# Performance work log

Hardware: AMD Instinct MI355X
Metric: run time of the kernel (lower is better)

Reference implementation:

```python
import jax, jax.numpy as jnp
import numpy as np

WS = 16                     # window_size
OW = 24                     # overlap_win_size = int(16*0.5)+16
PAD = (OW - WS) // 2        # unfold padding = 4
DIM = 384
HEADS = 6
HID = 768                   # mlp_ratio 2.0 * dim
TABLE = (WS + OW - 1) ** 2  # 1521


def _rel_pos_index():
    ch = np.arange(WS)
    coords = np.stack(np.meshgrid(ch, ch, indexing='ij')).reshape(2, -1)      # (2, WS*WS)
    co = np.arange(OW)
    coords_o = np.stack(np.meshgrid(co, co, indexing='ij')).reshape(2, -1)    # (2, OW*OW)
    rel = coords[:, :, None] - coords_o[:, None, :]                           # (2, nq, nk)
    rel = rel.transpose(1, 2, 0).astype(np.int64)
    rel[..., 0] += OW - 1
    rel[..., 1] += OW - 1
    rel[..., 0] *= WS + OW - 1
    return rel.sum(-1)                                                        # (WS*WS, OW*OW)

RPI = jnp.asarray(_rel_pos_index())


def _ln(x, g, b, eps=1e-5):
    m = x.mean(-1, keepdims=True)
    v = ((x - m) ** 2).mean(-1, keepdims=True)
    return (x - m) / jnp.sqrt(v + eps) * g + b


def _overlap_windows(t, H, W):
    # t: (B,H,W,C) -> (B*nw, OW*OW, C); overlapping patches, stride WS, pad PAD
    B, _, _, C = t.shape
    nH, nW = H // WS, W // WS
    tp = jnp.pad(t, ((0, 0), (PAD, PAD), (PAD, PAD), (0, 0)))
    r = (jnp.arange(nH) * WS)[:, None] + jnp.arange(OW)   # (nH, OW)
    c = (jnp.arange(nW) * WS)[:, None] + jnp.arange(OW)   # (nW, OW)
    p = tp[:, r]              # (B, nH, OW, Wp, C)
    p = p[:, :, :, c]         # (B, nH, OW, nW, OW, C)
    p = p.transpose(0, 1, 3, 2, 4, 5).reshape(B * nH * nW, OW * OW, C)
    return p


def setup_inputs() -> dict:
    key = jax.random.key(0)
    ks = jax.random.split(key, 8)
    H = W = 192
    B = 1
    inp = {
        'x': jax.random.normal(ks[0], (B, H * W, DIM), dtype=jnp.float32),
        'norm1_g': jnp.ones((DIM,), jnp.float32),
        'norm1_b': jnp.zeros((DIM,), jnp.float32),
        'qkv_w': jax.random.normal(ks[1], (DIM, 3 * DIM), jnp.float32) * 0.02,
        'qkv_b': jnp.zeros((3 * DIM,), jnp.float32),
        'rpb_table': jax.random.normal(ks[2], (TABLE, HEADS), jnp.float32) * 0.02,
        'proj_w': jax.random.normal(ks[3], (DIM, DIM), jnp.float32) * 0.02,
        'proj_b': jnp.zeros((DIM,), jnp.float32),
        'norm2_g': jnp.ones((DIM,), jnp.float32),
        'norm2_b': jnp.zeros((DIM,), jnp.float32),
        'fc1_w': jax.random.normal(ks[4], (DIM, HID), jnp.float32) * 0.02,
        'fc1_b': jnp.zeros((HID,), jnp.float32),
        'fc2_w': jax.random.normal(ks[5], (HID, DIM), jnp.float32) * 0.02,
        'fc2_b': jnp.zeros((DIM,), jnp.float32),
        'H': H,
        'W': W,
    }
    return inp


def reference(x, norm1_g, norm1_b, qkv_w, qkv_b, rpb_table, proj_w, proj_b,
              norm2_g, norm2_b, fc1_w, fc1_b, fc2_w, fc2_b, H, W):
    B, L, C = x.shape
    d = C // HEADS
    scale = d ** (-0.5)
    nH, nW = H // WS, W // WS

    shortcut = x
    xn = _ln(x, norm1_g, norm1_b).reshape(B, H, W, C)
    qkv = xn @ qkv_w + qkv_b                                   # (B,H,W,3C)
    q, k, v = qkv[..., :C], qkv[..., C:2 * C], qkv[..., 2 * C:]

    # non-overlapping query windows: (B*nw, WS*WS, C)
    qw = q.reshape(B, nH, WS, nW, WS, C).transpose(0, 1, 3, 2, 4, 5).reshape(-1, WS * WS, C)
    # overlapping key/value windows: (B*nw, OW*OW, C)
    kw = _overlap_windows(k, H, W)
    vw = _overlap_windows(v, H, W)

    b_ = qw.shape[0]
    qh = qw.reshape(b_, WS * WS, HEADS, d) * scale
    kh = kw.reshape(b_, OW * OW, HEADS, d)
    vh = vw.reshape(b_, OW * OW, HEADS, d)

    attn = jnp.einsum('bqhd,bkhd->bhqk', qh, kh)               # (b_, H, nq, nk)
    bias = rpb_table[RPI].transpose(2, 0, 1)                   # (heads, nq, nk)
    attn = jax.nn.softmax(attn + bias[None], axis=-1)
    out = jnp.einsum('bhqk,bkhd->bqhd', attn, vh).reshape(b_, WS * WS, C)

    # window reverse -> (B, H*W, C)
    out = out.reshape(B, nH, nW, WS, WS, C).transpose(0, 1, 3, 2, 4, 5).reshape(B, H * W, C)
    out = out @ proj_w + proj_b

    x = shortcut + out
    h = _ln(x, norm2_g, norm2_b)
    h = jax.nn.gelu(h @ fc1_w + fc1_b, approximate=False)
    h = h @ fc2_w + fc2_b
    return x + h
```

## Files before the change

kernel.cpp:

```cpp
#include <hip/hip_runtime.h>

#define LTOK 36864
#define DIMC 384
#define NHEADS 6
#define HDIM 64
#define HIDD 768
#define NWIN 12
#define WSZ 16
#define OWS 24
#define KVTOK 576

using bf16x8 = __attribute__((ext_vector_type(8))) short;
using f32x4  = __attribute__((ext_vector_type(4))) float;

__device__ inline unsigned short f2bf(float f) {
  unsigned u = __float_as_uint(f);
  return (unsigned short)((u + 0x7FFFu + ((u >> 16) & 1u)) >> 16);
}
__device__ inline float bf2f(unsigned short h) {
  return __uint_as_float(((unsigned)h) << 16);
}
__device__ __forceinline__ unsigned cvt_pk_bf16(float lo, float hi) {
  unsigned r;
  asm volatile("v_cvt_pk_bf16_f32 %0, %1, %2" : "=v"(r) : "v"(lo), "v"(hi));
  return r;
}
__device__ __forceinline__ unsigned short f2bf1(float x) {
  return (unsigned short)(cvt_pk_bf16(x, x) & 0xffffu);
}
__device__ __forceinline__ float fexp2(float x) {
#if __has_builtin(__builtin_amdgcn_exp2f)
  return __builtin_amdgcn_exp2f(x);
#else
  return exp2f(x);
#endif
}

typedef __attribute__((address_space(1))) const unsigned int GAS_U32;
typedef __attribute__((address_space(3))) unsigned int LAS_U32;
__device__ __forceinline__ void gl16(const void* g, void* l) {
  __builtin_amdgcn_global_load_lds((GAS_U32*)g, (LAS_U32*)l, 16, 0, 0);
}

__global__ void prep_kernel(const float* __restrict__ qkv_w, const float* __restrict__ proj_w,
                            const float* __restrict__ fc1_w, const float* __restrict__ fc2_w,
                            unsigned short* __restrict__ wq, unsigned short* __restrict__ wp,
                            unsigned short* __restrict__ w1, unsigned short* __restrict__ w2) {
  int id = blockIdx.x * 256 + threadIdx.x;
  if (id < 442368) {
    int n = id / 384, k = id - n * 384;
    wq[id] = f2bf(qkv_w[(size_t)k * 1152 + n]);
  } else if (id < 589824) {
    int i = id - 442368;
    int n = i / 384, k = i - n * 384;
    wp[i] = f2bf(proj_w[(size_t)k * 384 + n]);
  } else if (id < 884736) {
    int i = id - 589824;
    int n = i / 384, k = i - n * 384;
    w1[i] = f2bf(fc1_w[(size_t)k * 768 + n]);
  } else {
    int i = id - 884736;
    int n = i / 768, k = i - n * 768;
    w2[i] = f2bf(fc2_w[(size_t)k * 384 + n]);
  }
}

__global__ void rpb_expand_kernel(const float* __restrict__ rpb, float* __restrict__ biasm8) {
  int id = blockIdx.x * 256 + threadIdx.x;
  if (id >= NHEADS * 256 * 576) return;
  int head = id / 147456;
  int rem = id - head * 147456;
  int q = rem / 576;
  int kt = rem - q * 576;
  int ty = q >> 4, tx = q & 15;
  int oy = kt / 24, ox = kt - (kt / 24) * 24;
  biasm8[id] = rpb[((ty - oy + 23) * 39 + (tx - ox + 23)) * NHEADS + head] * 8.0f;
}

template <int BF16IN>
__global__ __launch_bounds__(256) void ln_kernel(const void* __restrict__ xv,
                                                 const float* __restrict__ g,
                                                 const float* __restrict__ b,
                                                 unsigned short* __restrict__ out) {
  int row = blockIdx.x * 4 + (threadIdx.x >> 6);
  int lane = threadIdx.x & 63;
  float v[6];
  float s = 0.f, ss = 0.f;
#pragma unroll
  for (int i = 0; i < 6; ++i) {
    int c = lane + i * 64;
    if (BF16IN) v[i] = bf2f(((const unsigned short*)xv)[(size_t)row * DIMC + c]);
    else        v[i] = ((const float*)xv)[(size_t)row * DIMC + c];
    s += v[i];
    ss += v[i] * v[i];
  }
#pragma unroll
  for (int off = 32; off; off >>= 1) {
    s += __shfl_xor(s, off);
    ss += __shfl_xor(ss, off);
  }
  float mean = s * (1.f / DIMC);
  float var = ss * (1.f / DIMC) - mean * mean;
  float rstd = rsqrtf(var + 1e-5f);
  unsigned short* outr = out + (size_t)row * DIMC;
#pragma unroll
  for (int i = 0; i < 6; ++i) {
    int c = lane + i * 64;
    outr[c] = f2bf((v[i] - mean) * rstd * g[c] + b[c]);
  }
}

template <int EPI>
__global__ __launch_bounds__(256) void gemm_bf16(const unsigned short* __restrict__ A,
                                                 const unsigned short* __restrict__ Bt,
                                                 const float* __restrict__ bias,
                                                 const void* __restrict__ residv,
                                                 void* __restrict__ outv,
                                                 int M, int N, int K) {
  __shared__ unsigned short As[3][4096];
  __shared__ unsigned short Bs[3][4096];
  const int tid = threadIdx.x;
  int id = blockIdx.y * gridDim.x + blockIdx.x;
  int chunk = (gridDim.x * gridDim.y) >> 3;
  int lid = (id & 7) * chunk + (id >> 3);
  const int m0 = (lid / gridDim.x) * 128;
  const int n0 = (lid % gridDim.x) * 128;
  const int lane = tid & 63;
  const int wave = tid >> 6;
  const int wr = wave >> 1;
  const int wc = wave & 1;
  const int l15 = lane & 15, l4 = lane >> 4;

  f32x4 acc[4][4];
#pragma unroll
  for (int i = 0; i < 4; ++i)
#pragma unroll
    for (int j = 0; j < 4; ++j) acc[i][j] = (f32x4){0.f, 0.f, 0.f, 0.f};

  const int srow = tid >> 2;
  const int scol = (tid & 3) << 3;
  const unsigned short* ga = A + (size_t)(m0 + srow) * K + scol;
  const unsigned short* gb = Bt + (size_t)(n0 + srow) * K + scol;

#define STAGE(buf, k0)                                        \
  do {                                                        \
    unsigned short* lA = As[buf] + wave * 512;                \
    unsigned short* lB = Bs[buf] + wave * 512;                \
    gl16(ga + (k0), lA);                                      \
    gl16(ga + (size_t)64 * K + (k0), lA + 2048);              \
    gl16(gb + (k0), lB);                                      \
    gl16(gb + (size_t)64 * K + (k0), lB + 2048);              \
  } while (0)

  const int nt = K >> 5;
  STAGE(0, 0);
  STAGE(1, 32);

  for (int t = 0; t < nt; ++t) {
    const int cur = t % 3;
    if (t + 1 < nt) {
      asm volatile("s_waitcnt vmcnt(4)" ::: "memory");
    } else {
      asm volatile("s_waitcnt vmcnt(0)" ::: "memory");
    }
    __builtin_amdgcn_s_barrier();

    if (t + 2 < nt) STAGE((t + 2) % 3, (t + 2) * 32);

    const unsigned short* arp = As[cur] + (wr * 64 + l15) * 32 + l4 * 8;
    const unsigned short* brp = Bs[cur] + (wc * 64 + l15) * 32 + l4 * 8;
    bf16x8 af[4], bfr[4];
#pragma unroll
    for (int i = 0; i < 4; ++i) af[i] = *(const bf16x8*)(arp + i * 512);
#pragma unroll
    for (int j = 0; j < 4; ++j) bfr[j] = *(const bf16x8*)(brp + j * 512);
#pragma unroll
    for (int i = 0; i < 4; ++i)
#pragma unroll
      for (int j = 0; j < 4; ++j)
        acc[i][j] = __builtin_amdgcn_mfma_f32_16x16x32_bf16(af[i], bfr[j], acc[i][j], 0, 0, 0);
  }
#undef STAGE

#pragma unroll
  for (int j = 0; j < 4; ++j) {
    int gcol = n0 + wc * 64 + j * 16 + l15;
    float bv = bias[gcol];
#pragma unroll
    for (int i = 0; i < 4; ++i) {
#pragma unroll
      for (int r = 0; r < 4; ++r) {
        int grow = m0 + wr * 64 + i * 16 + l4 * 4 + r;
        float v = acc[i][j][r] + bv;
        size_t idx = (size_t)grow * N + gcol;
        if (EPI == 0) {
          ((unsigned short*)outv)[idx] = f2bf(v);
        } else if (EPI == 2) {
          float gv = 0.5f * v * (1.f + erff(v * 0.70710678118654752f));
          ((unsigned short*)outv)[idx] = f2bf(gv);
        } else if (EPI == 3) {
          ((unsigned short*)outv)[idx] = f2bf(((const float*)residv)[idx] + v);
        } else {
          ((float*)outv)[idx] = bf2f(((const unsigned short*)residv)[idx]) + v;
        }
      }
    }
  }
}

__global__ __launch_bounds__(256, 3) void attn_kernel(const unsigned short* __restrict__ qkv,
                                                      const float* __restrict__ biasm8,
                                                      unsigned short* __restrict__ att) {
  __shared__ unsigned short ks[2][64][72];
  __shared__ unsigned short vts[2][64][72];
  __shared__ unsigned short pt[4][32][40];
  int bid = blockIdx.x;
  int lid = (bid & 7) * 216 + (bid >> 3);
  const int hw = lid >> 1;
  const int qh = lid & 1;
  const int win = hw / NHEADS;
  const int head = hw - win * NHEADS;
  const int wy = win / NWIN, wx = win - (win / NWIN) * NWIN;
  const int tid = threadIdx.x;
  const int w = tid >> 6, lane = tid & 63;
  const int l15 = lane & 15, l4 = lane >> 4;
  const float SC02 = 0.125f * 1.44269504f;
  const float C0 = -8.f * 1.44269504f;
  const bf16x8 ones = {(short)0x3F80, (short)0x3F80, (short)0x3F80, (short)0x3F80,
                       (short)0x3F80, (short)0x3F80, (short)0x3F80, (short)0x3F80};

  const int qrow0 = qh * 128 + w * 32;

  bf16x8 qf[2][2];
#pragma unroll
  for (int jq = 0; jq < 2; ++jq) {
    int q = qrow0 + jq * 16 + l15;
    int gy = wy * WSZ + (q >> 4), gx = wx * WSZ + (q & 15);
    const unsigned short* qp = qkv + (size_t)(gy * 192 + gx) * 1152 + head * HDIM + l4 * 8;
    qf[jq][0] = *(const bf16x8*)qp;
    qf[jq][1] = *(const bf16x8*)(qp + 32);
  }

  const float* bias_base = biasm8 + (size_t)head * 147456 + (size_t)(qrow0 + l15) * 576 + l4 * 4;

#define KS_W(buf, k0v, k1v)                          \
  do {                                               \
    *(uint4*)&ks[buf][lane][w * 16] = (k0v);         \
    *(uint4*)&ks[buf][lane][w * 16 + 8] = (k1v);     \
  } while (0)
#define VTS_W(buf, v0v, v1v)                                           \
  do {                                                                 \
    const unsigned short* vv = (const unsigned short*)&(v0v);          \
    _Pragma("unroll") for (int j = 0; j < 8; ++j)                      \
        vts[buf][w * 16 + j][lane] = vv[j];                            \
    vv = (const unsigned short*)&(v1v);                                \
    _Pragma("unroll") for (int j = 0; j < 8; ++j)                      \
        vts[buf][w * 16 + 8 + j][lane] = vv[j];                        \
  } while (0)

  {
    int kt = lane;
    int oy = kt / OWS, ox = kt - (kt / OWS) * OWS;
    int gy = wy * WSZ + oy - 4, gx = wx * WSZ + ox - 4;
    uint4 k0 = {0,0,0,0}, k1 = {0,0,0,0}, v0 = {0,0,0,0}, v1 = {0,0,0,0};
    if ((unsigned)gy < 192u && (unsigned)gx < 192u) {
      const unsigned short* gp = qkv + (size_t)(gy * 192 + gx) * 1152 + DIMC + head * HDIM + w * 16;
      k0 = *(const uint4*)gp;         k1 = *(const uint4*)(gp + 8);
      v0 = *(const uint4*)(gp + 384); v1 = *(const uint4*)(gp + 392);
    }
    KS_W(0, k0, k1);
    VTS_W(0, v0, v1);
  }

  f32x4 sacc[4][2];
#pragma unroll
  for (int i = 0; i < 4; ++i)
#pragma unroll
    for (int j2 = 0; j2 < 2; ++j2)
      sacc[i][j2] = *(const f32x4*)(bias_base + j2 * (16 * 576) + i * 16);

  __syncthreads();

  f32x4 oacc[2][4];
#pragma unroll
  for (int i = 0; i < 2; ++i)
#pragma unroll
    for (int j = 0; j < 4; ++j) oacc[i][j] = (f32x4){0.f, 0.f, 0.f, 0.f};
  f32x4 ol[2];
  ol[0] = (f32x4){0.f, 0.f, 0.f, 0.f};
  ol[1] = (f32x4){0.f, 0.f, 0.f, 0.f};

  for (int kb = 0; kb < 9; ++kb) {
    const int cur = kb & 1;
    const bool have = kb < 8;
    uint4 pk0 = {0,0,0,0}, pk1 = {0,0,0,0}, pv0 = {0,0,0,0}, pv1 = {0,0,0,0};
    if (have) {
      int kt = (kb + 1) * 64 + lane;
      int oy = kt / OWS, ox = kt - (kt / OWS) * OWS;
      int gy = wy * WSZ + oy - 4, gx = wx * WSZ + ox - 4;
      if ((unsigned)gy < 192u && (unsigned)gx < 192u) {
        const unsigned short* gp = qkv + (size_t)(gy * 192 + gx) * 1152 + DIMC + head * HDIM + w * 16;
        pk0 = *(const uint4*)gp;         pk1 = *(const uint4*)(gp + 8);
        pv0 = *(const uint4*)(gp + 384); pv1 = *(const uint4*)(gp + 392);
      }
    }

#pragma unroll
    for (int kk = 0; kk < 2; ++kk) {
      bf16x8 kf[4];
#pragma unroll
      for (int i = 0; i < 4; ++i)
        kf[i] = *(const bf16x8*)&ks[cur][i * 16 + l15][kk * 32 + l4 * 8];
      __builtin_amdgcn_s_setprio(1);
#pragma unroll
      for (int i = 0; i < 4; ++i)
#pragma unroll
        for (int j2 = 0; j2 < 2; ++j2)
          sacc[i][j2] = __builtin_amdgcn_mfma_f32_16x16x32_bf16(kf[i], qf[j2][kk], sacc[i][j2], 0, 0, 0);
      __builtin_amdgcn_s_setprio(0);
    }

#pragma unroll
    for (int i = 0; i < 4; ++i)
#pragma unroll
      for (int j2 = 0; j2 < 2; ++j2)
#pragma unroll
        for (int r = 0; r < 4; ++r)
          sacc[i][j2][r] = fexp2(fmaf(sacc[i][j2][r], SC02, C0));

#pragma unroll
    for (int kk = 0; kk < 2; ++kk) {
#pragma unroll
      for (int i2 = 0; i2 < 2; ++i2)
#pragma unroll
        for (int j2 = 0; j2 < 2; ++j2) {
          int i = kk * 2 + i2;
          uint2 pk;
          pk.x = cvt_pk_bf16(sacc[i][j2][0], sacc[i][j2][1]);
          pk.y = cvt_pk_bf16(sacc[i][j2][2], sacc[i][j2][3]);
          *(uint2*)&pt[w][j2 * 16 + l15][i2 * 16 + l4 * 4] = pk;
        }
      bf16x8 pf[2], vf[4];
#pragma unroll
      for (int j2 = 0; j2 < 2; ++j2)
        pf[j2] = *(const bf16x8*)&pt[w][j2 * 16 + l15][l4 * 8];
#pragma unroll
      for (int jd = 0; jd < 4; ++jd)
        vf[jd] = *(const bf16x8*)&vts[cur][jd * 16 + l15][kk * 32 + l4 * 8];
      __builtin_amdgcn_s_setprio(1);
#pragma unroll
      for (int j2 = 0; j2 < 2; ++j2) {
#pragma unroll
        for (int jd = 0; jd < 4; ++jd)
          oacc[j2][jd] = __builtin_amdgcn_mfma_f32_16x16x32_bf16(pf[j2], vf[jd], oacc[j2][jd], 0, 0, 0);
        ol[j2] = __builtin_amdgcn_mfma_f32_16x16x32_bf16(pf[j2], ones, ol[j2], 0, 0, 0);
      }
      __builtin_amdgcn_s_setprio(0);
    }

    if (have) {
      KS_W(cur ^ 1, pk0, pk1);
      VTS_W(cur ^ 1, pv0, pv1);
      const float* bp = bias_base + (kb + 1) * 64;
#pragma unroll
      for (int i = 0; i < 4; ++i)
#pragma unroll
        for (int j2 = 0; j2 < 2; ++j2)
          sacc[i][j2] = *(const f32x4*)(bp + j2 * (16 * 576) + i * 16);
    }
    __syncthreads();
  }
#undef KS_W
#undef VTS_W

#pragma unroll
  for (int j2 = 0; j2 < 2; ++j2) {
#pragma unroll
    for (int r = 0; r < 4; ++r) {
      float il = 1.f / ol[j2][r];
      int q = qrow0 + j2 * 16 + l4 * 4 + r;
      int gy = wy * WSZ + (q >> 4), gx = wx * WSZ + (q & 15);
      unsigned short* op = att + (size_t)(gy * 192 + gx) * DIMC + head * HDIM + l15;
#pragma unroll
      for (int jd = 0; jd < 4; ++jd) op[jd * 16] = f2bf1(oacc[j2][jd][r] * il);
    }
  }
}

extern "C" void kernel_launch(void* const* d_in, const int* in_sizes, int n_in,
                              void* d_out, int out_size, void* d_ws, size_t ws_size,
                              hipStream_t stream) {
  const float* x      = (const float*)d_in[0];
  const float* n1g    = (const float*)d_in[1];
  const float* n1b    = (const float*)d_in[2];
  const float* qkv_w  = (const float*)d_in[3];
  const float* qkv_b  = (const float*)d_in[4];
  const float* rpb    = (const float*)d_in[5];
  const float* proj_w = (const float*)d_in[6];
  const float* proj_b = (const float*)d_in[7];
  const float* n2g    = (const float*)d_in[8];
  const float* n2b    = (const float*)d_in[9];
  const float* fc1_w  = (const float*)d_in[10];
  const float* fc1_b  = (const float*)d_in[11];
  const float* fc2_w  = (const float*)d_in[12];
  const float* fc2_b  = (const float*)d_in[13];
  float* out = (float*)d_out;

  char* ws = (char*)d_ws;
  unsigned short* xn   = (unsigned short*)ws;
  unsigned short* qkvb = (unsigned short*)(ws + 28311552);
  unsigned short* xa   = (unsigned short*)(ws + 28311552 + 56623104);
  unsigned short* att  = (unsigned short*)(ws + 28311552 + 84934656);
  unsigned short* wq   = (unsigned short*)(ws + 141557760);
  unsigned short* wp   = wq + 1152 * 384;
  unsigned short* w1   = wp + 384 * 384;
  unsigned short* w2   = w1 + 768 * 384;
  float* biasm8 = (float*)ws;

  prep_kernel<<<4608, 256, 0, stream>>>(qkv_w, proj_w, fc1_w, fc2_w, wq, wp, w1, w2);

  ln_kernel<0><<<LTOK / 4, 256, 0, stream>>>(x, n1g, n1b, xn);
  gemm_bf16<0><<<dim3(1152 / 128, LTOK / 128), 256, 0, stream>>>(xn, wq, qkv_b, nullptr, qkvb,
                                                                 LTOK, 1152, DIMC);
  rpb_expand_kernel<<<(NHEADS * 256 * 576 + 255) / 256, 256, 0, stream>>>(rpb, biasm8);
  attn_kernel<<<dim3(NHEADS * 144 * 2), 256, 0, stream>>>(qkvb, biasm8, att);
  gemm_bf16<3><<<dim3(DIMC / 128, LTOK / 128), 256, 0, stream>>>(att, wp, proj_b, x, xa,
                                                                 LTOK, DIMC, DIMC);
  ln_kernel<1><<<LTOK / 4, 256, 0, stream>>>(xa, n2g, n2b, xn);
  gemm_bf16<2><<<dim3(HIDD / 128, LTOK / 128), 256, 0, stream>>>(xn, w1, fc1_b, nullptr, qkvb,
                                                                 LTOK, HIDD, DIMC);
  gemm_bf16<4><<<dim3(DIMC / 128, LTOK / 128), 256, 0, stream>>>(qkvb, w2, fc2_b, xa, out,
                                                                 LTOK, DIMC, HIDD);
}
```

Measured before the change: 317.6 us.

## Merge attention query halves into 512-thread blocks and tile weight transpose

Result: slower. 366.9 us (+15.5%).

```diff
diff --git a/kernel.cpp b/kernel.cpp
--- a/kernel.cpp
+++ b/kernel.cpp
@@ -13,10 +13,6 @@
 using bf16x8 = __attribute__((ext_vector_type(8))) short;
 using f32x4  = __attribute__((ext_vector_type(4))) float;
 
-__device__ inline unsigned short f2bf(float f) {
-  unsigned u = __float_as_uint(f);
-  return (unsigned short)((u + 0x7FFFu + ((u >> 16) & 1u)) >> 16);
-}
 __device__ inline float bf2f(unsigned short h) {
   return __uint_as_float(((unsigned)h) << 16);
 }
@@ -42,27 +38,35 @@
   __builtin_amdgcn_global_load_lds((GAS_U32*)g, (LAS_U32*)l, 16, 0, 0);
 }
 
-__global__ void prep_kernel(const float* __restrict__ qkv_w, const float* __restrict__ proj_w,
-                            const float* __restrict__ fc1_w, const float* __restrict__ fc2_w,
-                            unsigned short* __restrict__ wq, unsigned short* __restrict__ wp,
-                            unsigned short* __restrict__ w1, unsigned short* __restrict__ w2) {
-  int id = blockIdx.x * 256 + threadIdx.x;
-  if (id < 442368) {
-    int n = id / 384, k = id - n * 384;
-    wq[id] = f2bf(qkv_w[(size_t)k * 1152 + n]);
-  } else if (id < 589824) {
-    int i = id - 442368;
-    int n = i / 384, k = i - n * 384;
-    wp[i] = f2bf(proj_w[(size_t)k * 384 + n]);
-  } else if (id < 884736) {
-    int i = id - 589824;
-    int n = i / 384, k = i - n * 384;
-    w1[i] = f2bf(fc1_w[(size_t)k * 768 + n]);
-  } else {
-    int i = id - 884736;
-    int n = i / 768, k = i - n * 768;
-    w2[i] = f2bf(fc2_w[(size_t)k * 384 + n]);
-  }
+__global__ __launch_bounds__(256) void prep_kernel(const float* __restrict__ qkv_w,
+                                                   const float* __restrict__ proj_w,
+                                                   const float* __restrict__ fc1_w,
+                                                   const float* __restrict__ fc2_w,
+                                                   unsigned short* __restrict__ wq,
+                                                   unsigned short* __restrict__ wp,
+                                                   unsigned short* __restrict__ w1,
+                                                   unsigned short* __restrict__ w2) {
+  __shared__ float t[64][65];
+  int b = blockIdx.x;
+  const float* src;
+  unsigned short* dst;
+  int K, N, tb;
+  if (b < 108)      { src = qkv_w;  dst = wq; K = 384; N = 1152; tb = b; }
+  else if (b < 144) { src = proj_w; dst = wp; K = 384; N = 384;  tb = b - 108; }
+  else if (b < 216) { src = fc1_w;  dst = w1; K = 384; N = 768;  tb = b - 144; }
+  else              { src = fc2_w;  dst = w2; K = 768; N = 384;  tb = b - 216; }
+  int ntn = N >> 6;
+  int tk = tb / ntn, tn = tb - tk * ntn;
+  int r0 = tk << 6, c0 = tn << 6;
+  int rr = threadIdx.x >> 6;
+  int cc = threadIdx.x & 63;
+#pragma unroll
+  for (int i = 0; i < 16; ++i)
+    t[rr * 16 + i][cc] = src[(size_t)(r0 + rr * 16 + i) * N + c0 + cc];
+  __syncthreads();
+#pragma unroll
+  for (int i = 0; i < 16; ++i)
+    dst[(size_t)(c0 + rr * 16 + i) * K + r0 + cc] = f2bf1(t[cc][rr * 16 + i]);
 }
 
 __global__ void rpb_expand_kernel(const float* __restrict__ rpb, float* __restrict__ biasm8) {
@@ -106,7 +110,7 @@
 #pragma unroll
   for (int i = 0; i < 6; ++i) {
     int c = lane + i * 64;
-    outr[c] = f2bf((v[i] - mean) * rstd * g[c] + b[c]);
+    outr[c] = f2bf1((v[i] - mean) * rstd * g[c] + b[c]);
   }
 }
 
@@ -194,12 +198,12 @@
         float v = acc[i][j][r] + bv;
         size_t idx = (size_t)grow * N + gcol;
         if (EPI == 0) {
-          ((unsigned short*)outv)[idx] = f2bf(v);
+          ((unsigned short*)outv)[idx] = f2bf1(v);
         } else if (EPI == 2) {
           float gv = 0.5f * v * (1.f + erff(v * 0.70710678118654752f));
-          ((unsigned short*)outv)[idx] = f2bf(gv);
+          ((unsigned short*)outv)[idx] = f2bf1(gv);
         } else if (EPI == 3) {
-          ((unsigned short*)outv)[idx] = f2bf(((const float*)residv)[idx] + v);
+          ((unsigned short*)outv)[idx] = f2bf1(((const float*)residv)[idx] + v);
         } else {
           ((float*)outv)[idx] = bf2f(((const unsigned short*)residv)[idx]) + v;
         }
@@ -208,18 +212,16 @@
   }
 }
 
-__global__ __launch_bounds__(256, 3) void attn_kernel(const unsigned short* __restrict__ qkv,
+__global__ __launch_bounds__(512, 4) void attn_kernel(const unsigned short* __restrict__ qkv,
                                                       const float* __restrict__ biasm8,
                                                       unsigned short* __restrict__ att) {
   __shared__ unsigned short ks[2][64][72];
   __shared__ unsigned short vts[2][64][72];
-  __shared__ unsigned short pt[4][32][40];
+  __shared__ unsigned short pt[8][32][40];
   int bid = blockIdx.x;
-  int lid = (bid & 7) * 216 + (bid >> 3);
-  const int hw = lid >> 1;
-  const int qh = lid & 1;
-  const int win = hw / NHEADS;
-  const int head = hw - win * NHEADS;
+  int lid = (bid & 7) * 108 + (bid >> 3);
+  const int win = lid / NHEADS;
+  const int head = lid - win * NHEADS;
   const int wy = win / NWIN, wx = win - (win / NWIN) * NWIN;
   const int tid = threadIdx.x;
   const int w = tid >> 6, lane = tid & 63;
@@ -229,7 +231,7 @@
   const bf16x8 ones = {(short)0x3F80, (short)0x3F80, (short)0x3F80, (short)0x3F80,
                        (short)0x3F80, (short)0x3F80, (short)0x3F80, (short)0x3F80};
 
-  const int qrow0 = qh * 128 + w * 32;
+  const int qrow0 = w * 32;
 
   bf16x8 qf[2][2];
 #pragma unroll
@@ -243,33 +245,29 @@
 
   const float* bias_base = biasm8 + (size_t)head * 147456 + (size_t)(qrow0 + l15) * 576 + l4 * 4;
 
-#define KS_W(buf, k0v, k1v)                          \
-  do {                                               \
-    *(uint4*)&ks[buf][lane][w * 16] = (k0v);         \
-    *(uint4*)&ks[buf][lane][w * 16 + 8] = (k1v);     \
+#define KS_W(buf, k0v)                              \
+  do {                                              \
+    *(uint4*)&ks[buf][lane][w * 8] = (k0v);         \
   } while (0)
-#define VTS_W(buf, v0v, v1v)                                           \
+#define VTS_W(buf, v0v)                                                \
   do {                                                                 \
     const unsigned short* vv = (const unsigned short*)&(v0v);          \
     _Pragma("unroll") for (int j = 0; j < 8; ++j)                      \
-        vts[buf][w * 16 + j][lane] = vv[j];                            \
-    vv = (const unsigned short*)&(v1v);                                \
-    _Pragma("unroll") for (int j = 0; j < 8; ++j)                      \
-        vts[buf][w * 16 + 8 + j][lane] = vv[j];                        \
+        vts[buf][w * 8 + j][lane] = vv[j];                             \
   } while (0)
 
   {
     int kt = lane;
     int oy = kt / OWS, ox = kt - (kt / OWS) * OWS;
     int gy = wy * WSZ + oy - 4, gx = wx * WSZ + ox - 4;
-    uint4 k0 = {0,0,0,0}, k1 = {0,0,0,0}, v0 = {0,0,0,0}, v1 = {0,0,0,0};
+    uint4 k0 = {0,0,0,0}, v0 = {0,0,0,0};
     if ((unsigned)gy < 192u && (unsigned)gx < 192u) {
-      const unsigned short* gp = qkv + (size_t)(gy * 192 + gx) * 1152 + DIMC + head * HDIM + w * 16;
-      k0 = *(const uint4*)gp;         k1 = *(const uint4*)(gp + 8);
-      v0 = *(const uint4*)(gp + 384); v1 = *(const uint4*)(gp + 392);
-    }
-    KS_W(0, k0, k1);
-    VTS_W(0, v0, v1);
+      const unsigned short* gp = qkv + (size_t)(gy * 192 + gx) * 1152 + DIMC + head * HDIM + w * 8;
+      k0 = *(const uint4*)gp;
+      v0 = *(const uint4*)(gp + 384);
+    }
+    KS_W(0, k0);
+    VTS_W(0, v0);
   }
 
   f32x4 sacc[4][2];
@@ -293,15 +291,15 @@
   for (int kb = 0; kb < 9; ++kb) {
     const int cur = kb & 1;
     const bool have = kb < 8;
-    uint4 pk0 = {0,0,0,0}, pk1 = {0,0,0,0}, pv0 = {0,0,0,0}, pv1 = {0,0,0,0};
+    uint4 pk0 = {0,0,0,0}, pv0 = {0,0,0,0};
     if (have) {
       int kt = (kb + 1) * 64 + lane;
       int oy = kt / OWS, ox = kt - (kt / OWS) * OWS;
       int gy = wy * WSZ + oy - 4, gx = wx * WSZ + ox - 4;
       if ((unsigned)gy < 192u && (unsigned)gx < 192u) {
-        const unsigned short* gp = qkv + (size_t)(gy * 192 + gx) * 1152 + DIMC + head * HDIM + w * 16;
-        pk0 = *(const uint4*)gp;         pk1 = *(const uint4*)(gp + 8);
-        pv0 = *(const uint4*)(gp + 384); pv1 = *(const uint4*)(gp + 392);
+        const unsigned short* gp = qkv + (size_t)(gy * 192 + gx) * 1152 + DIMC + head * HDIM + w * 8;
+        pk0 = *(const uint4*)gp;
+        pv0 = *(const uint4*)(gp + 384);
       }
     }
 
@@ -359,8 +357,8 @@
     }
 
     if (have) {
-      KS_W(cur ^ 1, pk0, pk1);
-      VTS_W(cur ^ 1, pv0, pv1);
+      KS_W(cur ^ 1, pk0);
+      VTS_W(cur ^ 1, pv0);
       const float* bp = bias_base + (kb + 1) * 64;
 #pragma unroll
       for (int i = 0; i < 4; ++i)
@@ -417,13 +415,13 @@
   unsigned short* w2   = w1 + 768 * 384;
   float* biasm8 = (float*)ws;
 
-  prep_kernel<<<4608, 256, 0, stream>>>(qkv_w, proj_w, fc1_w, fc2_w, wq, wp, w1, w2);
+  prep_kernel<<<288, 256, 0, stream>>>(qkv_w, proj_w, fc1_w, fc2_w, wq, wp, w1, w2);
 
   ln_kernel<0><<<LTOK / 4, 256, 0, stream>>>(x, n1g, n1b, xn);
   gemm_bf16<0><<<dim3(1152 / 128, LTOK / 128), 256, 0, stream>>>(xn, wq, qkv_b, nullptr, qkvb,
                                                                  LTOK, 1152, DIMC);
   rpb_expand_kernel<<<(NHEADS * 256 * 576 + 255) / 256, 256, 0, stream>>>(rpb, biasm8);
-  attn_kernel<<<dim3(NHEADS * 144 * 2), 256, 0, stream>>>(qkvb, biasm8, att);
+  attn_kernel<<<dim3(NHEADS * 144), 512, 0, stream>>>(qkvb, biasm8, att);
   gemm_bf16<3><<<dim3(DIMC / 128, LTOK / 128), 256, 0, stream>>>(att, wp, proj_b, x, xa,
                                                                  LTOK, DIMC, DIMC);
   ln_kernel<1><<<LTOK / 4, 256, 0, stream>>>(xa, n2g, n2b, xn);
```
